# Kernel tuning notes

Hardware: AMD Instinct MI355X
Metric: run time of the kernel (lower is better)

The kernel has to match this reference:

```python
import jax, jax.numpy as jnp
import numpy as np

N_NODES = 100_000
N_EDGES = 1_000_000
IN_CH = 32
EDGE_CH = 16
OUT_CH = 32
D_CAT = 2 * IN_CH + EDGE_CH  # 80
D_MID = 56                   # linspace(80, 32, 3)[1]


def setup_inputs() -> dict:
    key = jax.random.key(0)
    ks = jax.random.split(key, 8)
    x = jax.random.normal(ks[0], (N_NODES, IN_CH), dtype=jnp.float32)
    edge_index = jax.random.randint(ks[1], (2, N_EDGES), 0, N_NODES, dtype=jnp.int64)
    edge_attr = jax.random.normal(ks[2], (N_EDGES, EDGE_CH), dtype=jnp.float32)
    # MLP params: Linear(80->56), Linear(56->32), bias=True (homogeneous_flag=False)
    W1 = jax.random.normal(ks[3], (D_CAT, D_MID), dtype=jnp.float32) / np.sqrt(D_CAT).astype(np.float32)
    b1 = jnp.zeros((D_MID,), dtype=jnp.float32)
    W2 = jax.random.normal(ks[4], (D_MID, OUT_CH), dtype=jnp.float32) / np.sqrt(D_MID).astype(np.float32)
    b2 = jnp.zeros((OUT_CH,), dtype=jnp.float32)
    return {"x": x, "edge_index": edge_index, "edge_attr": edge_attr,
            "W1": W1, "b1": b1, "W2": W2, "b2": b2}


def reference(x, edge_index, edge_attr, W1, b1, W2, b2):
    num_nodes = x.shape[0]
    rol, col = edge_index[0], edge_index[1]
    # gather node pairs + concat edge features: [E, 2*in + edge]
    e = jnp.concatenate([x[rol], x[col], edge_attr], axis=-1)
    # edge MLP (LeakyReLU after every layer, as in IterGNN's MLP)
    h = jax.nn.leaky_relu(e @ W1 + b1)
    v = jax.nn.leaky_relu(h @ W2 + b2)  # [E, out]
    # Max aggregation by destination node (scatter-max); empty segments -> 0
    agg = jax.ops.segment_max(v, col, num_segments=num_nodes)
    agg = jnp.where(jnp.isneginf(agg), jnp.zeros((), dtype=agg.dtype), agg)
    # elementwise max with trailing slice of input features
    out = jnp.maximum(agg, x[:, -v.shape[-1]:])
    return out
```

## Files before the change

### kernel.cpp

```cpp
#include <hip/hip_runtime.h>

#define N_NODES 100000
#define IN_CH 32
#define EDGE_CH 16
#define OUT_CH 32
#define D_CAT 80
#define D_MID 56

#define BKT_SHIFT 6
#define BKT_NODES 64
#define NB 1563
#define NB_ALL 1568
#define CAP 1024

#define NSUP 196
#define CAP_SUP 5632
#define K1_EDGES 2048
#define K1_EPT 4
#define K2_SPLIT 4
#define K2_SLICE 1408
#define K2_SITERS 3

#define EPB 256
#define NT_E 16

#define W1F_SH 4096
#define W2F_SH 2048
#define W1D_SH 2048
#define WIMG_SH (W1F_SH + W2F_SH + W1D_SH)
#define FEATF_SH (NT_E * 2 * 64 * 8)

#define HSTRIDE 68
#define AGG_LD 33
#define ENC_NEGINF 0x007FFFFFu

typedef short short8 __attribute__((ext_vector_type(8)));
typedef float f32x4 __attribute__((ext_vector_type(4)));
typedef int i32x2 __attribute__((ext_vector_type(2)));

#define WS_IMG    0
#define WS_B1     16384
#define WS_B2     16640
#define WS_SUPCNT 16768
#define WS_GCNT   17664
#define WS_Z0     16768
#define WS_ZSZ    (17664 + 6272 - 16768)
#define WS_SUPREC 24576
#define WS_REC    8855552
#define WS_XB_A   21700608
#define XB_BYTES  6400000
#define WS_NEED_A ((size_t)WS_XB_A)
#define WS_NEED_AX ((size_t)WS_XB_A + XB_BYTES)
#define WS_XB_B   12869632
#define WS_NEED_B ((size_t)WS_XB_B)
#define WS_NEED_BX ((size_t)WS_XB_B + XB_BYTES)

__device__ __forceinline__ unsigned fenc(float f) {
    unsigned u = __float_as_uint(f);
    return (u & 0x80000000u) ? ~u : (u | 0x80000000u);
}
__device__ __forceinline__ float fdec(unsigned u) {
    u = (u & 0x80000000u) ? (u ^ 0x80000000u) : ~u;
    return __uint_as_float(u);
}
__device__ __forceinline__ float bfr(float f) {
    unsigned u = __float_as_uint(f);
    u = (u + 0x7FFFu + ((u >> 16) & 1u)) & 0xFFFF0000u;
    return __uint_as_float(u);
}
__device__ __forceinline__ unsigned short bf16b(float f) {
    unsigned u = __float_as_uint(f);
    return (unsigned short)((u + 0x7FFFu + ((u >> 16) & 1u)) >> 16);
}
__device__ __forceinline__ short8 cvt8(float4 a, float4 b) {
    return short8{ (short)bf16b(a.x), (short)bf16b(a.y), (short)bf16b(a.z), (short)bf16b(a.w),
                   (short)bf16b(b.x), (short)bf16b(b.y), (short)bf16b(b.z), (short)bf16b(b.w) };
}

__device__ __forceinline__ void convert_x_bf16(const float* __restrict__ x,
                                               unsigned short* __restrict__ xb,
                                               int gtid, int gstride) {
    const int tot = N_NODES * IN_CH / 8;
    for (int i = gtid; i < tot; i += gstride) {
        float4 a = ((const float4*)x)[2 * i];
        float4 b = ((const float4*)x)[2 * i + 1];
        *(short8*)&xb[i * 8] = cvt8(a, b);
    }
}

__device__ void build_weight_image(const float* __restrict__ W1, const float* __restrict__ b1,
                                   const float* __restrict__ W2, const float* __restrict__ b2,
                                   unsigned short* __restrict__ wsImg,
                                   float* __restrict__ wsb1, float* __restrict__ wsb2,
                                   int t, int nthr) {
    for (int s = t; s < W1F_SH; s += nthr) {
        int j = s & 7, l = (s >> 3) & 63, fi = s >> 9;
        int nt = fi & 3, ks = fi >> 2;
        int n = nt * 16 + (l & 15), kl = ks * 32 + (l >> 4) * 8 + j;
        unsigned short v = 0;
        if (n < D_MID) {
            if (kl < 32) v = bf16b(W1[kl * D_MID + n]);
            else if (kl < 48) v = bf16b(W1[(64 + kl - 32) * D_MID + n]);
        }
        wsImg[s] = v;
    }
    for (int s = t; s < W2F_SH; s += nthr) {
        int j = s & 7, l = (s >> 3) & 63, fi = s >> 9;
        int nt = fi & 1, ks = fi >> 1;
        int n = nt * 16 + (l & 15), kl = ks * 32 + (l >> 4) * 8 + j;
        wsImg[W1F_SH + s] = (kl < D_MID) ? bf16b(W2[kl * OUT_CH + n]) : (unsigned short)0;
    }
    for (int s = t; s < W1D_SH; s += nthr) {
        int j = s & 7, l = (s >> 3) & 63, fi = s >> 9;
        int nt = fi & 3;
        int n = nt * 16 + (l & 15), kl = (l >> 4) * 8 + j;
        wsImg[W1F_SH + W2F_SH + s] = (n < D_MID) ? bf16b(W1[(32 + kl) * D_MID + n]) : (unsigned short)0;
    }
    if (t < 64) wsb1[t] = (t < D_MID) ? bfr(b1[t]) : 0.f;
    else if (t < 96) wsb2[t - 64] = bfr(b2[t - 64]);
}

__global__ __launch_bounds__(512) void coarse_bin(
    const int* __restrict__ ei, int nE, int* __restrict__ gSupCnt, int2* __restrict__ supRec,
    const float* __restrict__ W1, const float* __restrict__ b1,
    const float* __restrict__ W2, const float* __restrict__ b2,
    unsigned short* __restrict__ wsImg, float* __restrict__ wsb1, float* __restrict__ wsb2)
{
    __shared__ int cnt[256], wb[256], cur[256];
    const int t = threadIdx.x;
    if (blockIdx.x == 0) build_weight_image(W1, b1, W2, b2, wsImg, wsb1, wsb2, t, 512);
    if (t < 256) cnt[t] = 0;
    __syncthreads();

    const int lo = blockIdx.x * K1_EDGES;
    int rdst[K1_EPT], rsrc[K1_EPT];
#pragma unroll
    for (int k = 0; k < K1_EPT; ++k) {
        int e = lo + k * 512 + t;
        bool v = e < nE;
        rdst[k] = v ? __builtin_nontemporal_load(ei + nE + e) : -1;
        rsrc[k] = v ? __builtin_nontemporal_load(ei + e) : 0;
        if ((unsigned)rdst[k] >= N_NODES) rdst[k] = -1;
        if ((unsigned)rsrc[k] >= N_NODES) rsrc[k] = 0;
        if (rdst[k] >= 0) atomicAdd(&cnt[rdst[k] >> 9], 1);
    }
    __syncthreads();
    if (t < 256) {
        int c = cnt[t];
        wb[t] = c ? atomicAdd(&gSupCnt[t], c) : 0;
        cur[t] = 0;
    }
    __syncthreads();
#pragma unroll
    for (int k = 0; k < K1_EPT; ++k) {
        if (rdst[k] >= 0) {
            int s = rdst[k] >> 9;
            int pos = wb[s] + atomicAdd(&cur[s], 1);
            if (pos < CAP_SUP) {
                int e = lo + k * 512 + t;
                supRec[(size_t)s * CAP_SUP + pos] =
                    make_int2(rsrc[k], ((rdst[k] & 511) << 20) | e);
            }
        }
    }
}

__global__ __launch_bounds__(512) void fine_bin(
    const int* __restrict__ gSupCnt, const int2* __restrict__ supRec,
    int* __restrict__ gCnt, int2* __restrict__ rec,
    const float* __restrict__ x, unsigned short* __restrict__ xb)
{
    const int blk = blockIdx.x;
    const int s = blk >> 2, sl = blk & (K2_SPLIT - 1);
    const int t = threadIdx.x, lane = t & 63;

    if (xb) convert_x_bf16(x, xb, blk * 512 + t, NSUP * K2_SPLIT * 512);

    const int cntS = min(gSupCnt[s], CAP_SUP);
    const int lo = sl * K2_SLICE;
    const int hi = min(cntS, lo + K2_SLICE);

    int2 r[K2_SITERS];
#pragma unroll
    for (int k = 0; k < K2_SITERS; ++k) {
        int i = lo + k * 512 + t;
        r[k] = (i < hi) ? supRec[(size_t)s * CAP_SUP + i] : make_int2(0, 0);
    }
#pragma unroll
    for (int k = 0; k < K2_SITERS; ++k) {
        int i = lo + k * 512 + t;
        bool v = i < hi;
        int f = v ? ((r[k].y >> 26) & 7) : -1;
        int rank = 0, wbase = 0;
#pragma unroll
        for (int vv = 0; vv < 8; ++vv) {
            unsigned long long m = __ballot(f == vv);
            if (lane == vv) wbase = m ? atomicAdd(&gCnt[s * 8 + vv], (int)__popcll(m)) : 0;
            if (f == vv) rank = (int)__popcll(m & ((1ull << lane) - 1ull));
        }
        int base = __shfl(wbase, f & 7);
        if (v) {
            int pos = base + rank;
            if (pos < CAP)
                rec[(size_t)(s * 8 + f) * CAP + pos] =
                    make_int2(r[k].x, (((r[k].y >> 20) & 63) << 20) | (r[k].y & 0xFFFFF));
        }
    }
}

__global__ __launch_bounds__(512) void scatter_append(
    const int* __restrict__ ei, int* __restrict__ gCnt, int2* __restrict__ rec, int nE,
    const float* __restrict__ W1, const float* __restrict__ b1,
    const float* __restrict__ W2, const float* __restrict__ b2,
    unsigned short* __restrict__ wsImg, float* __restrict__ wsb1, float* __restrict__ wsb2,
    const float* __restrict__ x, unsigned short* __restrict__ xb)
{
    __shared__ int lh[NB];
    __shared__ int lbase[NB];
    if (blockIdx.x == 0) build_weight_image(W1, b1, W2, b2, wsImg, wsb1, wsb2, threadIdx.x, 512);
    if (xb) convert_x_bf16(x, xb, blockIdx.x * 512 + threadIdx.x, gridDim.x * 512);
    for (int i = threadIdx.x; i < NB; i += 512) lh[i] = 0;
    __syncthreads();
    int per = (nE + gridDim.x - 1) / gridDim.x;
    int lo = blockIdx.x * per;
    int hi = min(lo + per, nE);
    for (int e = lo + threadIdx.x; e < hi; e += 512) {
        int dst = __builtin_nontemporal_load(ei + nE + e);
        if ((unsigned)dst < N_NODES) atomicAdd(&lh[dst >> BKT_SHIFT], 1);
    }
    __syncthreads();
    for (int i = threadIdx.x; i < NB; i += 512) {
        int c = lh[i];
        lbase[i] = c ? atomicAdd(&gCnt[i], c) : 0;
        lh[i] = 0;
    }
    __syncthreads();
    for (int e = lo + threadIdx.x; e < hi; e += 512) {
        int dst = __builtin_nontemporal_load(ei + nE + e);
        if ((unsigned)dst >= N_NODES) continue;
        int b = dst >> BKT_SHIFT;
        int p = lbase[b] + atomicAdd(&lh[b], 1);
        if (p >= CAP) continue;
        int src = __builtin_nontemporal_load(ei + e);
        if ((unsigned)src >= N_NODES) src = 0;
        rec[(size_t)b * CAP + p] = make_int2(src, ((dst & (BKT_NODES - 1)) << 20) | e);
    }
}

template<int XB>
__global__ __launch_bounds__(512, 4) void bucket_mlp(
    const float* __restrict__ x, const unsigned short* __restrict__ xb,
    const float* __restrict__ ea,
    const int2* __restrict__ rec, const int* __restrict__ gCnt,
    const unsigned short* __restrict__ wsImg,
    const float* __restrict__ wsb1, const float* __restrict__ wsb2,
    float* __restrict__ out)
{
    __shared__ unsigned short sFeatF[FEATF_SH];
    __shared__ unsigned short sWgt[WIMG_SH];
    __shared__ float sHdst[BKT_NODES * HSTRIDE];
    __shared__ unsigned aggL[BKT_NODES * AGG_LD];
    __shared__ float sb1f[64];
    __shared__ float sb2f[32];
    __shared__ int sdl[EPB];

    unsigned short* const sW1F = sWgt;
    unsigned short* const sW2F = sWgt + W1F_SH;
    unsigned short* const sW1D = sWgt + W1F_SH + W2F_SH;
    unsigned short* const sHF  = sFeatF;

    const int t = threadIdx.x;
    const int nodeBase = blockIdx.x << BKT_SHIFT;
    const int base = blockIdx.x * CAP;
    const int cnt  = min(gCnt[blockIdx.x], CAP);

    for (int i = t; i < WIMG_SH / 8; i += 512)
        *(short8*)&sWgt[i * 8] = *(const short8*)(wsImg + i * 8);
    for (int i = t; i < BKT_NODES * AGG_LD; i += 512) aggL[i] = ENC_NEGINF;
    if (t < 64) sb1f[t] = wsb1[t];
    else if (t < 96) sb2f[t - 64] = wsb2[t - 64];

    const int wave = t >> 6;
    const int l15  = t & 15;
    const int quad = (t & 63) >> 4;
    const int lane = t & 63;
    const int slot = t >> 1, q = t & 1;
    const int sl15 = slot & 15, set = slot >> 4;

    short8 rv16[4];
    int rdl;

    auto loadRec = [&](int idx) -> i32x2 {
        return (idx < cnt) ? *(const i32x2*)(rec + base + idx) : (i32x2){0, 0};
    };
    auto gather = [&](i32x2 r2, bool ok) {
        rdl = ok ? ((r2.y >> 20) & 63) : -1;
        short8 z = {0, 0, 0, 0, 0, 0, 0, 0};
        if (q == 0) {
            if constexpr (XB) {
                const short8* xs8 = (const short8*)(xb + (size_t)r2.x * IN_CH);
#pragma unroll
                for (int k = 0; k < 4; ++k) rv16[k] = ok ? xs8[k] : z;
            } else {
                const float* xs = x + (size_t)r2.x * IN_CH;
#pragma unroll
                for (int k = 0; k < 4; ++k)
                    rv16[k] = ok ? cvt8(((const float4*)xs)[2 * k], ((const float4*)xs)[2 * k + 1]) : z;
            }
        } else {
            const float* ep = ea + (size_t)(r2.y & 0xFFFFF) * EDGE_CH;
#pragma unroll
            for (int k = 0; k < 2; ++k)
                rv16[k] = ok ? cvt8(((const float4*)ep)[2 * k], ((const float4*)ep)[2 * k + 1]) : z;
            rv16[2] = z; rv16[3] = z;
        }
    };
    auto storeChunk = [&]() {
        if (q == 0) sdl[slot] = rdl;
#pragma unroll
        for (int k = 0; k < 4; ++k) {
            int cj = q * 4 + k;
            int a16 = (set * 2 + (cj >> 2)) * 64 + (cj & 3) * 16 + sl15;
            *(short8*)&sFeatF[a16 * 8] = rv16[k];
        }
    };

    i32x2 recC = loadRec(slot);
    i32x2 recN = loadRec(EPB + slot);
    gather(recC, slot < cnt);

    __syncthreads();

    {
        const int ntile = wave & 3, mh = wave >> 2;
        int node = nodeBase + ntile * 16 + l15;
        short8 bfr8 = {0, 0, 0, 0, 0, 0, 0, 0};
        if (node < N_NODES) {
            if constexpr (XB) {
                bfr8 = *(const short8*)(xb + (size_t)node * IN_CH + quad * 8);
            } else {
                const float* xp = x + (size_t)node * IN_CH + quad * 8;
                bfr8 = cvt8(((const float4*)xp)[0], ((const float4*)xp)[1]);
            }
        }
        f32x4 accd[2] = {(f32x4){0.f, 0.f, 0.f, 0.f}, (f32x4){0.f, 0.f, 0.f, 0.f}};
#pragma unroll
        for (int i = 0; i < 2; ++i) {
            int nt = mh * 2 + i;
            short8 af = *(const short8*)&sW1D[(nt * 64 + lane) * 8];
            accd[i] = __builtin_amdgcn_mfma_f32_16x16x32_bf16(af, bfr8, accd[i], 0, 0, 0);
        }
#pragma unroll
        for (int i = 0; i < 2; ++i) {
            int nt = mh * 2 + i, c0 = nt * 16 + quad * 4;
            float4 vv;
#pragma unroll
            for (int j = 0; j < 4; ++j) {
                int c = c0 + j;
                ((float*)&vv)[j] = (c < D_MID) ? accd[i][j] + sb1f[c] : 0.f;
            }
            *(float4*)&sHdst[(ntile * 16 + l15) * HSTRIDE + c0] = vv;
        }
    }

    for (int c0e = 0; c0e < cnt; c0e += EPB) {
        storeChunk();
        __syncthreads();
        gather(recN, (c0e + EPB + slot) < cnt);
        recN = loadRec(c0e + 2 * EPB + slot);

        f32x4 acc[2][4];
#pragma unroll
        for (int ei = 0; ei < 2; ++ei)
#pragma unroll
            for (int nt = 0; nt < 4; ++nt) acc[ei][nt] = (f32x4){0.f, 0.f, 0.f, 0.f};
#pragma unroll
        for (int ks = 0; ks < 2; ++ks) {
            short8 bf0 = *(const short8*)&sFeatF[((wave * 2 + ks) * 64 + lane) * 8];
            short8 bf1 = *(const short8*)&sFeatF[(((wave + 8) * 2 + ks) * 64 + lane) * 8];
#pragma unroll
            for (int nt = 0; nt < 4; ++nt) {
                short8 af = *(const short8*)&sW1F[((ks * 4 + nt) * 64 + lane) * 8];
                acc[0][nt] = __builtin_amdgcn_mfma_f32_16x16x32_bf16(af, bf0, acc[0][nt], 0, 0, 0);
                acc[1][nt] = __builtin_amdgcn_mfma_f32_16x16x32_bf16(af, bf1, acc[1][nt], 0, 0, 0);
            }
        }
        __syncthreads();

#pragma unroll
        for (int ei = 0; ei < 2; ++ei) {
            int et = wave + ei * 8;
            int dl = sdl[et * 16 + l15];
            const float* hrow = &sHdst[((dl >= 0) ? dl : 0) * HSTRIDE];
#pragma unroll
            for (int nt = 0; nt < 4; ++nt) {
                int c0 = nt * 16 + quad * 4;
                float4 hd = *(const float4*)&hrow[c0];
                int ks2 = nt >> 1;
                int quad2 = (nt * 2 + (quad >> 1)) & 3;
                int off = (quad & 1) * 4;
                ushort4 p;
#pragma unroll
                for (int j = 0; j < 4; ++j) {
                    float v = acc[ei][nt][j] + ((const float*)&hd)[j];
                    v = (v > 0.f) ? v : 0.01f * v;
                    ((unsigned short*)&p)[j] = (c0 + j < D_MID) ? bf16b(v) : (unsigned short)0;
                }
                *(ushort4*)&sHF[((et * 2 + ks2) * 64 + quad2 * 16 + l15) * 8 + off] = p;
            }
        }
        __syncthreads();

        f32x4 acc2[2][2];
#pragma unroll
        for (int ei = 0; ei < 2; ++ei)
#pragma unroll
            for (int nt = 0; nt < 2; ++nt) acc2[ei][nt] = (f32x4){0.f, 0.f, 0.f, 0.f};
#pragma unroll
        for (int ks = 0; ks < 2; ++ks) {
            short8 bf0 = *(const short8*)&sHF[((wave * 2 + ks) * 64 + lane) * 8];
            short8 bf1 = *(const short8*)&sHF[(((wave + 8) * 2 + ks) * 64 + lane) * 8];
#pragma unroll
            for (int nt = 0; nt < 2; ++nt) {
                short8 af = *(const short8*)&sW2F[((ks * 2 + nt) * 64 + lane) * 8];
                acc2[0][nt] = __builtin_amdgcn_mfma_f32_16x16x32_bf16(af, bf0, acc2[0][nt], 0, 0, 0);
                acc2[1][nt] = __builtin_amdgcn_mfma_f32_16x16x32_bf16(af, bf1, acc2[1][nt], 0, 0, 0);
            }
        }

#pragma unroll
        for (int ei = 0; ei < 2; ++ei) {
            int et = wave + ei * 8;
            int dl = sdl[et * 16 + l15];
            if (dl >= 0) {
                unsigned* arow = &aggL[dl * AGG_LD];
#pragma unroll
                for (int nt = 0; nt < 2; ++nt) {
                    int c0 = nt * 16 + quad * 4;
#pragma unroll
                    for (int j = 0; j < 4; ++j) {
                        float v = acc2[ei][nt][j] + sb2f[c0 + j];
                        v = (v > 0.f) ? v : 0.01f * v;
                        atomicMax(arow + c0 + j, fenc(bfr(v)));
                    }
                }
            }
        }
        __syncthreads();
    }
    __syncthreads();

    {
        int nl = t >> 3, g4 = t & 7;
        int node = nodeBase + nl;
        if (node < N_NODES) {
            const unsigned* ar = &aggL[nl * AGG_LD + g4 * 4];
            float4 o;
            if constexpr (XB) {
                ushort4 xw = ((const ushort4*)(xb + (size_t)node * IN_CH))[g4];
                o.x = fmaxf((ar[0] == ENC_NEGINF) ? 0.f : fdec(ar[0]), __uint_as_float((unsigned)xw.x << 16));
                o.y = fmaxf((ar[1] == ENC_NEGINF) ? 0.f : fdec(ar[1]), __uint_as_float((unsigned)xw.y << 16));
                o.z = fmaxf((ar[2] == ENC_NEGINF) ? 0.f : fdec(ar[2]), __uint_as_float((unsigned)xw.z << 16));
                o.w = fmaxf((ar[3] == ENC_NEGINF) ? 0.f : fdec(ar[3]), __uint_as_float((unsigned)xw.w << 16));
            } else {
                float4 xv = ((const float4*)(x + (size_t)node * IN_CH))[g4];
                o.x = fmaxf((ar[0] == ENC_NEGINF) ? 0.f : fdec(ar[0]), bfr(xv.x));
                o.y = fmaxf((ar[1] == ENC_NEGINF) ? 0.f : fdec(ar[1]), bfr(xv.y));
                o.z = fmaxf((ar[2] == ENC_NEGINF) ? 0.f : fdec(ar[2]), bfr(xv.z));
                o.w = fmaxf((ar[3] == ENC_NEGINF) ? 0.f : fdec(ar[3]), bfr(xv.w));
            }
            ((float4*)(out + (size_t)node * OUT_CH))[g4] = o;
        }
    }
}

extern "C" void kernel_launch(void* const* d_in, const int* in_sizes, int n_in,
                              void* d_out, int out_size, void* d_ws, size_t ws_size,
                              hipStream_t stream) {
    const float* x  = (const float*)d_in[0];
    const int*   ei = (const int*)d_in[1];
    const float* ea = (const float*)d_in[2];
    const float* W1 = (const float*)d_in[3];
    const float* b1 = (const float*)d_in[4];
    const float* W2 = (const float*)d_in[5];
    const float* b2 = (const float*)d_in[6];

    char* ws = (char*)d_ws;
    unsigned short* wsImg = (unsigned short*)(ws + WS_IMG);
    float* wsb1 = (float*)(ws + WS_B1);
    float* wsb2 = (float*)(ws + WS_B2);
    int* gSupCnt = (int*)(ws + WS_SUPCNT);
    int* gCnt = (int*)(ws + WS_GCNT);

    const int nE = in_sizes[1] / 2;
    float* out = (float*)d_out;

    if (ws_size >= WS_NEED_A) {
        int2* supRec = (int2*)(ws + WS_SUPREC);
        int2* rec    = (int2*)(ws + WS_REC);
        bool xbOn = ws_size >= WS_NEED_AX;
        unsigned short* xb = xbOn ? (unsigned short*)(ws + WS_XB_A) : nullptr;
        hipMemsetAsync(ws + WS_Z0, 0, WS_ZSZ, stream);
        coarse_bin<<<(nE + K1_EDGES - 1) / K1_EDGES, 512, 0, stream>>>(
            ei, nE, gSupCnt, supRec, W1, b1, W2, b2, wsImg, wsb1, wsb2);
        fine_bin<<<NSUP * K2_SPLIT, 512, 0, stream>>>(gSupCnt, supRec, gCnt, rec, x, xb);
        if (xbOn)
            bucket_mlp<1><<<NB, 512, 0, stream>>>(x, xb, ea, rec, gCnt, wsImg, wsb1, wsb2, out);
        else
            bucket_mlp<0><<<NB, 512, 0, stream>>>(x, nullptr, ea, rec, gCnt, wsImg, wsb1, wsb2, out);
    } else {
        int2* rec = (int2*)(ws + 24576);
        bool xbOn = ws_size >= WS_NEED_BX;
        unsigned short* xb = xbOn ? (unsigned short*)(ws + WS_XB_B) : nullptr;
        hipMemsetAsync(gCnt, 0, NB_ALL * sizeof(int), stream);
        scatter_append<<<128, 512, 0, stream>>>(ei, gCnt, rec, nE, W1, b1, W2, b2,
                                                wsImg, wsb1, wsb2, x, xb);
        if (xbOn)
            bucket_mlp<1><<<NB, 512, 0, stream>>>(x, xb, ea, rec, gCnt, wsImg, wsb1, wsb2, out);
        else
            bucket_mlp<0><<<NB, 512, 0, stream>>>(x, nullptr, ea, rec, gCnt, wsImg, wsb1, wsb2, out);
    }
}
```

Before: 225.2 us.

## Fuse edge binning and bucket MLP into one cooperative kernel with grid sync

Adds a cooperative kernel that first bins edges into destination buckets with block-local histograms and global atomics. After a grid-wide sync, the same persistent blocks loop over the buckets and run the bf16 MFMA edge MLP with scatter-max aggregation. The launcher tries this path first and falls back to the old multi-kernel pipelines if the cooperative launch fails. This removes the separate coarse and fine binning passes and the inter-kernel launch gaps. In exchange it relies on a fixed grid of 512 persistent blocks, adds grid-sync cost, and gives up the two-level binning's write locality.

```diff
diff --git a/kernel.cpp b/kernel.cpp
--- a/kernel.cpp
+++ b/kernel.cpp
@@ -1,4 +1,7 @@
 #include <hip/hip_runtime.h>
+#include <hip/hip_cooperative_groups.h>
+
+namespace cg = cooperative_groups;
 
 #define N_NODES 100000
 #define IN_CH 32
@@ -20,6 +23,8 @@
 #define K2_SPLIT 4
 #define K2_SLICE 1408
 #define K2_SITERS 3
+
+#define COOP_GRID 512
 
 #define EPB 256
 #define NT_E 16
@@ -120,6 +125,281 @@
     else if (t < 96) wsb2[t - 64] = bfr(b2[t - 64]);
 }
 
+template<int XB>
+__global__ __launch_bounds__(512, 4) void fused_all(
+    const float* __restrict__ x, unsigned short* __restrict__ xb,
+    const float* __restrict__ ea, const int* __restrict__ ei, int nE,
+    int* __restrict__ gCnt, int2* __restrict__ rec,
+    const float* __restrict__ W1, const float* __restrict__ b1,
+    const float* __restrict__ W2, const float* __restrict__ b2,
+    unsigned short* __restrict__ wsImg, float* __restrict__ wsb1, float* __restrict__ wsb2,
+    float* __restrict__ out)
+{
+    __shared__ unsigned short sFeatF[FEATF_SH];
+    __shared__ unsigned short sWgt[WIMG_SH];
+    __shared__ float sHdst[BKT_NODES * HSTRIDE];
+    __shared__ unsigned aggL[BKT_NODES * AGG_LD];
+    __shared__ float sb1f[64];
+    __shared__ float sb2f[32];
+    __shared__ int sdl[EPB];
+
+    const int t = threadIdx.x;
+    const int blk = blockIdx.x, nblk = gridDim.x;
+
+    {
+        int* const lh = (int*)sFeatF;
+        int* const lbase = ((int*)sFeatF) + NB;
+        if (blk == 0) build_weight_image(W1, b1, W2, b2, wsImg, wsb1, wsb2, t, 512);
+        if constexpr (XB) convert_x_bf16(x, xb, blk * 512 + t, nblk * 512);
+        for (int i = t; i < NB; i += 512) lh[i] = 0;
+        __syncthreads();
+
+        const int per = (nE + nblk - 1) / nblk;
+        const int lo = blk * per, hi = min(lo + per, nE);
+        int rdst[4], rsrc[4];
+#pragma unroll
+        for (int k = 0; k < 4; ++k) {
+            int e = lo + k * 512 + t;
+            bool v = e < hi;
+            rdst[k] = v ? __builtin_nontemporal_load(ei + nE + e) : -1;
+            rsrc[k] = v ? __builtin_nontemporal_load(ei + e) : 0;
+            if ((unsigned)rdst[k] >= N_NODES) rdst[k] = -1;
+            if ((unsigned)rsrc[k] >= N_NODES) rsrc[k] = 0;
+            if (rdst[k] >= 0) atomicAdd(&lh[rdst[k] >> BKT_SHIFT], 1);
+        }
+        __syncthreads();
+        for (int i = t; i < NB; i += 512) {
+            int c = lh[i];
+            lbase[i] = c ? atomicAdd(&gCnt[i], c) : 0;
+            lh[i] = 0;
+        }
+        __syncthreads();
+#pragma unroll
+        for (int k = 0; k < 4; ++k) {
+            if (rdst[k] >= 0) {
+                int b = rdst[k] >> BKT_SHIFT;
+                int p = lbase[b] + atomicAdd(&lh[b], 1);
+                if (p < CAP) {
+                    int e = lo + k * 512 + t;
+                    rec[(size_t)b * CAP + p] = make_int2(rsrc[k], ((rdst[k] & 63) << 20) | e);
+                }
+            }
+        }
+    }
+
+    cg::this_grid().sync();
+
+    unsigned short* const sW1F = sWgt;
+    unsigned short* const sW2F = sWgt + W1F_SH;
+    unsigned short* const sW1D = sWgt + W1F_SH + W2F_SH;
+    unsigned short* const sHF  = sFeatF;
+
+    for (int i = t; i < WIMG_SH / 8; i += 512)
+        *(short8*)&sWgt[i * 8] = *(const short8*)(wsImg + i * 8);
+    if (t < 64) sb1f[t] = wsb1[t];
+    else if (t < 96) sb2f[t - 64] = wsb2[t - 64];
+
+    const int wave = t >> 6;
+    const int l15  = t & 15;
+    const int quad = (t & 63) >> 4;
+    const int lane = t & 63;
+    const int slot = t >> 1, q = t & 1;
+    const int sl15 = slot & 15, set = slot >> 4;
+
+    for (int b = blk; b < NB; b += nblk) {
+        const int nodeBase = b << BKT_SHIFT;
+        const int base = b * CAP;
+        const int cnt  = min(gCnt[b], CAP);
+
+        __syncthreads();
+        for (int i = t; i < BKT_NODES * AGG_LD; i += 512) aggL[i] = ENC_NEGINF;
+
+        short8 rv16[4];
+        int rdl;
+        auto loadRec = [&](int idx) -> i32x2 {
+            return (idx < cnt) ? *(const i32x2*)(rec + base + idx) : (i32x2){0, 0};
+        };
+        auto gather = [&](i32x2 r2, bool ok) {
+            rdl = ok ? ((r2.y >> 20) & 63) : -1;
+            short8 z = {0, 0, 0, 0, 0, 0, 0, 0};
+            if (q == 0) {
+                if constexpr (XB) {
+                    const short8* xs8 = (const short8*)(xb + (size_t)r2.x * IN_CH);
+#pragma unroll
+                    for (int k = 0; k < 4; ++k) rv16[k] = ok ? xs8[k] : z;
+                } else {
+                    const float* xs = x + (size_t)r2.x * IN_CH;
+#pragma unroll
+                    for (int k = 0; k < 4; ++k)
+                        rv16[k] = ok ? cvt8(((const float4*)xs)[2 * k], ((const float4*)xs)[2 * k + 1]) : z;
+                }
+            } else {
+                const float* ep = ea + (size_t)(r2.y & 0xFFFFF) * EDGE_CH;
+#pragma unroll
+                for (int k = 0; k < 2; ++k)
+                    rv16[k] = ok ? cvt8(((const float4*)ep)[2 * k], ((const float4*)ep)[2 * k + 1]) : z;
+                rv16[2] = z; rv16[3] = z;
+            }
+        };
+        auto storeChunk = [&]() {
+            if (q == 0) sdl[slot] = rdl;
+#pragma unroll
+            for (int k = 0; k < 4; ++k) {
+                int cj = q * 4 + k;
+                int a16 = (set * 2 + (cj >> 2)) * 64 + (cj & 3) * 16 + sl15;
+                *(short8*)&sFeatF[a16 * 8] = rv16[k];
+            }
+        };
+
+        i32x2 recC = loadRec(slot);
+        i32x2 recN = loadRec(EPB + slot);
+        gather(recC, slot < cnt);
+
+        {
+            const int ntile = wave & 3, mh = wave >> 2;
+            int node = nodeBase + ntile * 16 + l15;
+            short8 bfr8 = {0, 0, 0, 0, 0, 0, 0, 0};
+            if (node < N_NODES) {
+                if constexpr (XB) {
+                    bfr8 = *(const short8*)(xb + (size_t)node * IN_CH + quad * 8);
+                } else {
+                    const float* xp = x + (size_t)node * IN_CH + quad * 8;
+                    bfr8 = cvt8(((const float4*)xp)[0], ((const float4*)xp)[1]);
+                }
+            }
+            f32x4 accd[2] = {(f32x4){0.f, 0.f, 0.f, 0.f}, (f32x4){0.f, 0.f, 0.f, 0.f}};
+#pragma unroll
+            for (int i = 0; i < 2; ++i) {
+                int nt = mh * 2 + i;
+                short8 af = *(const short8*)&sW1D[(nt * 64 + lane) * 8];
+                accd[i] = __builtin_amdgcn_mfma_f32_16x16x32_bf16(af, bfr8, accd[i], 0, 0, 0);
+            }
+#pragma unroll
+            for (int i = 0; i < 2; ++i) {
+                int nt = mh * 2 + i, c0 = nt * 16 + quad * 4;
+                float4 vv;
+#pragma unroll
+                for (int j = 0; j < 4; ++j) {
+                    int c = c0 + j;
+                    ((float*)&vv)[j] = (c < D_MID) ? accd[i][j] + sb1f[c] : 0.f;
+                }
+                *(float4*)&sHdst[(ntile * 16 + l15) * HSTRIDE + c0] = vv;
+            }
+        }
+
+        for (int c0e = 0; c0e < cnt; c0e += EPB) {
+            storeChunk();
+            __syncthreads();
+            gather(recN, (c0e + EPB + slot) < cnt);
+            recN = loadRec(c0e + 2 * EPB + slot);
+
+            f32x4 acc[2][4];
+#pragma unroll
+            for (int ei2 = 0; ei2 < 2; ++ei2)
+#pragma unroll
+                for (int nt = 0; nt < 4; ++nt) acc[ei2][nt] = (f32x4){0.f, 0.f, 0.f, 0.f};
+#pragma unroll
+            for (int ks = 0; ks < 2; ++ks) {
+                short8 bf0 = *(const short8*)&sFeatF[((wave * 2 + ks) * 64 + lane) * 8];
+                short8 bf1 = *(const short8*)&sFeatF[(((wave + 8) * 2 + ks) * 64 + lane) * 8];
+#pragma unroll
+                for (int nt = 0; nt < 4; ++nt) {
+                    short8 af = *(const short8*)&sW1F[((ks * 4 + nt) * 64 + lane) * 8];
+                    acc[0][nt] = __builtin_amdgcn_mfma_f32_16x16x32_bf16(af, bf0, acc[0][nt], 0, 0, 0);
+                    acc[1][nt] = __builtin_amdgcn_mfma_f32_16x16x32_bf16(af, bf1, acc[1][nt], 0, 0, 0);
+                }
+            }
+            __syncthreads();
+
+#pragma unroll
+            for (int ei2 = 0; ei2 < 2; ++ei2) {
+                int et = wave + ei2 * 8;
+                int dl = sdl[et * 16 + l15];
+                const float* hrow = &sHdst[((dl >= 0) ? dl : 0) * HSTRIDE];
+#pragma unroll
+                for (int nt = 0; nt < 4; ++nt) {
+                    int c0 = nt * 16 + quad * 4;
+                    float4 hd = *(const float4*)&hrow[c0];
+                    int ks2 = nt >> 1;
+                    int quad2 = (nt * 2 + (quad >> 1)) & 3;
+                    int off = (quad & 1) * 4;
+                    ushort4 p;
+#pragma unroll
+                    for (int j = 0; j < 4; ++j) {
+                        float v = acc[ei2][nt][j] + ((const float*)&hd)[j];
+                        v = (v > 0.f) ? v : 0.01f * v;
+                        ((unsigned short*)&p)[j] = (c0 + j < D_MID) ? bf16b(v) : (unsigned short)0;
+                    }
+                    *(ushort4*)&sHF[((et * 2 + ks2) * 64 + quad2 * 16 + l15) * 8 + off] = p;
+                }
+            }
+            __syncthreads();
+
+            f32x4 acc2[2][2];
+#pragma unroll
+            for (int ei2 = 0; ei2 < 2; ++ei2)
+#pragma unroll
+                for (int nt = 0; nt < 2; ++nt) acc2[ei2][nt] = (f32x4){0.f, 0.f, 0.f, 0.f};
+#pragma unroll
+            for (int ks = 0; ks < 2; ++ks) {
+                short8 bf0 = *(const short8*)&sHF[((wave * 2 + ks) * 64 + lane) * 8];
+                short8 bf1 = *(const short8*)&sHF[(((wave + 8) * 2 + ks) * 64 + lane) * 8];
+#pragma unroll
+                for (int nt = 0; nt < 2; ++nt) {
+                    short8 af = *(const short8*)&sW2F[((ks * 2 + nt) * 64 + lane) * 8];
+                    acc2[0][nt] = __builtin_amdgcn_mfma_f32_16x16x32_bf16(af, bf0, acc2[0][nt], 0, 0, 0);
+                    acc2[1][nt] = __builtin_amdgcn_mfma_f32_16x16x32_bf16(af, bf1, acc2[1][nt], 0, 0, 0);
+                }
+            }
+
+#pragma unroll
+            for (int ei2 = 0; ei2 < 2; ++ei2) {
+                int et = wave + ei2 * 8;
+                int dl = sdl[et * 16 + l15];
+                if (dl >= 0) {
+                    unsigned* arow = &aggL[dl * AGG_LD];
+#pragma unroll
+                    for (int nt = 0; nt < 2; ++nt) {
+                        int c0 = nt * 16 + quad * 4;
+#pragma unroll
+                        for (int j = 0; j < 4; ++j) {
+                            float v = acc2[ei2][nt][j] + sb2f[c0 + j];
+                            v = (v > 0.f) ? v : 0.01f * v;
+                            atomicMax(arow + c0 + j, fenc(bfr(v)));
+                        }
+                    }
+                }
+            }
+            __syncthreads();
+        }
+        __syncthreads();
+
+        {
+            int nl = t >> 3, g4 = t & 7;
+            int node = nodeBase + nl;
+            if (node < N_NODES) {
+                const unsigned* ar = &aggL[nl * AGG_LD + g4 * 4];
+                float4 o;
+                if constexpr (XB) {
+                    ushort4 xw = ((const ushort4*)(xb + (size_t)node * IN_CH))[g4];
+                    o.x = fmaxf((ar[0] == ENC_NEGINF) ? 0.f : fdec(ar[0]), __uint_as_float((unsigned)xw.x << 16));
+                    o.y = fmaxf((ar[1] == ENC_NEGINF) ? 0.f : fdec(ar[1]), __uint_as_float((unsigned)xw.y << 16));
+                    o.z = fmaxf((ar[2] == ENC_NEGINF) ? 0.f : fdec(ar[2]), __uint_as_float((unsigned)xw.z << 16));
+                    o.w = fmaxf((ar[3] == ENC_NEGINF) ? 0.f : fdec(ar[3]), __uint_as_float((unsigned)xw.w << 16));
+                } else {
+                    float4 xv = ((const float4*)(x + (size_t)node * IN_CH))[g4];
+                    o.x = fmaxf((ar[0] == ENC_NEGINF) ? 0.f : fdec(ar[0]), bfr(xv.x));
+                    o.y = fmaxf((ar[1] == ENC_NEGINF) ? 0.f : fdec(ar[1]), bfr(xv.y));
+                    o.z = fmaxf((ar[2] == ENC_NEGINF) ? 0.f : fdec(ar[2]), bfr(xv.z));
+                    o.w = fmaxf((ar[3] == ENC_NEGINF) ? 0.f : fdec(ar[3]), bfr(xv.w));
+                }
+                ((float4*)(out + (size_t)node * OUT_CH))[g4] = o;
+            }
+        }
+    }
+}
+
+
 __global__ __launch_bounds__(512) void coarse_bin(
     const int* __restrict__ ei, int nE, int* __restrict__ gSupCnt, int2* __restrict__ supRec,
     const float* __restrict__ W1, const float* __restrict__ b1,
@@ -204,6 +484,233 @@
             if (pos < CAP)
                 rec[(size_t)(s * 8 + f) * CAP + pos] =
                     make_int2(r[k].x, (((r[k].y >> 20) & 63) << 20) | (r[k].y & 0xFFFFF));
+        }
+    }
+}
+
+template<int XB>
+__global__ __launch_bounds__(512, 4) void bucket_mlp(
+    const float* __restrict__ x, const unsigned short* __restrict__ xb,
+    const float* __restrict__ ea,
+    const int2* __restrict__ rec, const int* __restrict__ gCnt,
+    const unsigned short* __restrict__ wsImg,
+    const float* __restrict__ wsb1, const float* __restrict__ wsb2,
+    float* __restrict__ out)
+{
+    __shared__ unsigned short sFeatF[FEATF_SH];
+    __shared__ unsigned short sWgt[WIMG_SH];
+    __shared__ float sHdst[BKT_NODES * HSTRIDE];
+    __shared__ unsigned aggL[BKT_NODES * AGG_LD];
+    __shared__ float sb1f[64];
+    __shared__ float sb2f[32];
+    __shared__ int sdl[EPB];
+
+    unsigned short* const sW1F = sWgt;
+    unsigned short* const sW2F = sWgt + W1F_SH;
+    unsigned short* const sW1D = sWgt + W1F_SH + W2F_SH;
+    unsigned short* const sHF  = sFeatF;
+
+    const int t = threadIdx.x;
+    const int nodeBase = blockIdx.x << BKT_SHIFT;
+    const int base = blockIdx.x * CAP;
+    const int cnt  = min(gCnt[blockIdx.x], CAP);
+
+    for (int i = t; i < WIMG_SH / 8; i += 512)
+        *(short8*)&sWgt[i * 8] = *(const short8*)(wsImg + i * 8);
+    for (int i = t; i < BKT_NODES * AGG_LD; i += 512) aggL[i] = ENC_NEGINF;
+    if (t < 64) sb1f[t] = wsb1[t];
+    else if (t < 96) sb2f[t - 64] = wsb2[t - 64];
+
+    const int wave = t >> 6;
+    const int l15  = t & 15;
+    const int quad = (t & 63) >> 4;
+    const int lane = t & 63;
+    const int slot = t >> 1, q = t & 1;
+    const int sl15 = slot & 15, set = slot >> 4;
+
+    short8 rv16[4];
+    int rdl;
+
+    auto loadRec = [&](int idx) -> i32x2 {
+        return (idx < cnt) ? *(const i32x2*)(rec + base + idx) : (i32x2){0, 0};
+    };
+    auto gather = [&](i32x2 r2, bool ok) {
+        rdl = ok ? ((r2.y >> 20) & 63) : -1;
+        short8 z = {0, 0, 0, 0, 0, 0, 0, 0};
+        if (q == 0) {
+            if constexpr (XB) {
+                const short8* xs8 = (const short8*)(xb + (size_t)r2.x * IN_CH);
+#pragma unroll
+                for (int k = 0; k < 4; ++k) rv16[k] = ok ? xs8[k] : z;
+            } else {
+                const float* xs = x + (size_t)r2.x * IN_CH;
+#pragma unroll
+                for (int k = 0; k < 4; ++k)
+                    rv16[k] = ok ? cvt8(((const float4*)xs)[2 * k], ((const float4*)xs)[2 * k + 1]) : z;
+            }
+        } else {
+            const float* ep = ea + (size_t)(r2.y & 0xFFFFF) * EDGE_CH;
+#pragma unroll
+            for (int k = 0; k < 2; ++k)
+                rv16[k] = ok ? cvt8(((const float4*)ep)[2 * k], ((const float4*)ep)[2 * k + 1]) : z;
+            rv16[2] = z; rv16[3] = z;
+        }
+    };
+    auto storeChunk = [&]() {
+        if (q == 0) sdl[slot] = rdl;
+#pragma unroll
+        for (int k = 0; k < 4; ++k) {
+            int cj = q * 4 + k;
+            int a16 = (set * 2 + (cj >> 2)) * 64 + (cj & 3) * 16 + sl15;
+            *(short8*)&sFeatF[a16 * 8] = rv16[k];
+        }
+    };
+
+    i32x2 recC = loadRec(slot);
+    i32x2 recN = loadRec(EPB + slot);
+    gather(recC, slot < cnt);
+
+    __syncthreads();
+
+    {
+        const int ntile = wave & 3, mh = wave >> 2;
+        int node = nodeBase + ntile * 16 + l15;
+        short8 bfr8 = {0, 0, 0, 0, 0, 0, 0, 0};
+        if (node < N_NODES) {
+            if constexpr (XB) {
+                bfr8 = *(const short8*)(xb + (size_t)node * IN_CH + quad * 8);
+            } else {
+                const float* xp = x + (size_t)node * IN_CH + quad * 8;
+                bfr8 = cvt8(((const float4*)xp)[0], ((const float4*)xp)[1]);
+            }
+        }
+        f32x4 accd[2] = {(f32x4){0.f, 0.f, 0.f, 0.f}, (f32x4){0.f, 0.f, 0.f, 0.f}};
+#pragma unroll
+        for (int i = 0; i < 2; ++i) {
+            int nt = mh * 2 + i;
+            short8 af = *(const short8*)&sW1D[(nt * 64 + lane) * 8];
+            accd[i] = __builtin_amdgcn_mfma_f32_16x16x32_bf16(af, bfr8, accd[i], 0, 0, 0);
+        }
+#pragma unroll
+        for (int i = 0; i < 2; ++i) {
+            int nt = mh * 2 + i, c0 = nt * 16 + quad * 4;
+            float4 vv;
+#pragma unroll
+            for (int j = 0; j < 4; ++j) {
+                int c = c0 + j;
+                ((float*)&vv)[j] = (c < D_MID) ? accd[i][j] + sb1f[c] : 0.f;
+            }
+            *(float4*)&sHdst[(ntile * 16 + l15) * HSTRIDE + c0] = vv;
+        }
+    }
+
+    for (int c0e = 0; c0e < cnt; c0e += EPB) {
+        storeChunk();
+        __syncthreads();
+        gather(recN, (c0e + EPB + slot) < cnt);
+        recN = loadRec(c0e + 2 * EPB + slot);
+
+        f32x4 acc[2][4];
+#pragma unroll
+        for (int ei2 = 0; ei2 < 2; ++ei2)
+#pragma unroll
+            for (int nt = 0; nt < 4; ++nt) acc[ei2][nt] = (f32x4){0.f, 0.f, 0.f, 0.f};
+#pragma unroll
+        for (int ks = 0; ks < 2; ++ks) {
+            short8 bf0 = *(const short8*)&sFeatF[((wave * 2 + ks) * 64 + lane) * 8];
+            short8 bf1 = *(const short8*)&sFeatF[(((wave + 8) * 2 + ks) * 64 + lane) * 8];
+#pragma unroll
+            for (int nt = 0; nt < 4; ++nt) {
+                short8 af = *(const short8*)&sW1F[((ks * 4 + nt) * 64 + lane) * 8];
+                acc[0][nt] = __builtin_amdgcn_mfma_f32_16x16x32_bf16(af, bf0, acc[0][nt], 0, 0, 0);
+                acc[1][nt] = __builtin_amdgcn_mfma_f32_16x16x32_bf16(af, bf1, acc[1][nt], 0, 0, 0);
+            }
+        }
+        __syncthreads();
+
+#pragma unroll
+        for (int ei2 = 0; ei2 < 2; ++ei2) {
+            int et = wave + ei2 * 8;
+            int dl = sdl[et * 16 + l15];
+            const float* hrow = &sHdst[((dl >= 0) ? dl : 0) * HSTRIDE];
+#pragma unroll
+            for (int nt = 0; nt < 4; ++nt) {
+                int c0 = nt * 16 + quad * 4;
+                float4 hd = *(const float4*)&hrow[c0];
+                int ks2 = nt >> 1;
+                int quad2 = (nt * 2 + (quad >> 1)) & 3;
+                int off = (quad & 1) * 4;
+                ushort4 p;
+#pragma unroll
+                for (int j = 0; j < 4; ++j) {
+                    float v = acc[ei2][nt][j] + ((const float*)&hd)[j];
+                    v = (v > 0.f) ? v : 0.01f * v;
+                    ((unsigned short*)&p)[j] = (c0 + j < D_MID) ? bf16b(v) : (unsigned short)0;
+                }
+                *(ushort4*)&sHF[((et * 2 + ks2) * 64 + quad2 * 16 + l15) * 8 + off] = p;
+            }
+        }
+        __syncthreads();
+
+        f32x4 acc2[2][2];
+#pragma unroll
+        for (int ei2 = 0; ei2 < 2; ++ei2)
+#pragma unroll
+            for (int nt = 0; nt < 2; ++nt) acc2[ei2][nt] = (f32x4){0.f, 0.f, 0.f, 0.f};
+#pragma unroll
+        for (int ks = 0; ks < 2; ++ks) {
+            short8 bf0 = *(const short8*)&sHF[((wave * 2 + ks) * 64 + lane) * 8];
+            short8 bf1 = *(const short8*)&sHF[(((wave + 8) * 2 + ks) * 64 + lane) * 8];
+#pragma unroll
+            for (int nt = 0; nt < 2; ++nt) {
+                short8 af = *(const short8*)&sW2F[((ks * 2 + nt) * 64 + lane) * 8];
+                acc2[0][nt] = __builtin_amdgcn_mfma_f32_16x16x32_bf16(af, bf0, acc2[0][nt], 0, 0, 0);
+                acc2[1][nt] = __builtin_amdgcn_mfma_f32_16x16x32_bf16(af, bf1, acc2[1][nt], 0, 0, 0);
+            }
+        }
+
+#pragma unroll
+        for (int ei2 = 0; ei2 < 2; ++ei2) {
+            int et = wave + ei2 * 8;
+            int dl = sdl[et * 16 + l15];
+            if (dl >= 0) {
+                unsigned* arow = &aggL[dl * AGG_LD];
+#pragma unroll
+                for (int nt = 0; nt < 2; ++nt) {
+                    int c0 = nt * 16 + quad * 4;
+#pragma unroll
+                    for (int j = 0; j < 4; ++j) {
+                        float v = acc2[ei2][nt][j] + sb2f[c0 + j];
+                        v = (v > 0.f) ? v : 0.01f * v;
+                        atomicMax(arow + c0 + j, fenc(bfr(v)));
+                    }
+                }
+            }
+        }
+        __syncthreads();
+    }
+    __syncthreads();
+
+    {
+        int nl = t >> 3, g4 = t & 7;
+        int node = nodeBase + nl;
+        if (node < N_NODES) {
+            const unsigned* ar = &aggL[nl * AGG_LD + g4 * 4];
+            float4 o;
+            if constexpr (XB) {
+                ushort4 xw = ((const ushort4*)(xb + (size_t)node * IN_CH))[g4];
+                o.x = fmaxf((ar[0] == ENC_NEGINF) ? 0.f : fdec(ar[0]), __uint_as_float((unsigned)xw.x << 16));
+                o.y = fmaxf((ar[1] == ENC_NEGINF) ? 0.f : fdec(ar[1]), __uint_as_float((unsigned)xw.y << 16));
+                o.z = fmaxf((ar[2] == ENC_NEGINF) ? 0.f : fdec(ar[2]), __uint_as_float((unsigned)xw.z << 16));
+                o.w = fmaxf((ar[3] == ENC_NEGINF) ? 0.f : fdec(ar[3]), __uint_as_float((unsigned)xw.w << 16));
+            } else {
+                float4 xv = ((const float4*)(x + (size_t)node * IN_CH))[g4];
+                o.x = fmaxf((ar[0] == ENC_NEGINF) ? 0.f : fdec(ar[0]), bfr(xv.x));
+                o.y = fmaxf((ar[1] == ENC_NEGINF) ? 0.f : fdec(ar[1]), bfr(xv.y));
+                o.z = fmaxf((ar[2] == ENC_NEGINF) ? 0.f : fdec(ar[2]), bfr(xv.z));
+                o.w = fmaxf((ar[3] == ENC_NEGINF) ? 0.f : fdec(ar[3]), bfr(xv.w));
+            }
+            ((float4*)(out + (size_t)node * OUT_CH))[g4] = o;
         }
     }
 }
@@ -247,233 +754,6 @@
     }
 }
 
-template<int XB>
-__global__ __launch_bounds__(512, 4) void bucket_mlp(
-    const float* __restrict__ x, const unsigned short* __restrict__ xb,
-    const float* __restrict__ ea,
-    const int2* __restrict__ rec, const int* __restrict__ gCnt,
-    const unsigned short* __restrict__ wsImg,
-    const float* __restrict__ wsb1, const float* __restrict__ wsb2,
-    float* __restrict__ out)
-{
-    __shared__ unsigned short sFeatF[FEATF_SH];
-    __shared__ unsigned short sWgt[WIMG_SH];
-    __shared__ float sHdst[BKT_NODES * HSTRIDE];
-    __shared__ unsigned aggL[BKT_NODES * AGG_LD];
-    __shared__ float sb1f[64];
-    __shared__ float sb2f[32];
-    __shared__ int sdl[EPB];
-
-    unsigned short* const sW1F = sWgt;
-    unsigned short* const sW2F = sWgt + W1F_SH;
-    unsigned short* const sW1D = sWgt + W1F_SH + W2F_SH;
-    unsigned short* const sHF  = sFeatF;
-
-    const int t = threadIdx.x;
-    const int nodeBase = blockIdx.x << BKT_SHIFT;
-    const int base = blockIdx.x * CAP;
-    const int cnt  = min(gCnt[blockIdx.x], CAP);
-
-    for (int i = t; i < WIMG_SH / 8; i += 512)
-        *(short8*)&sWgt[i * 8] = *(const short8*)(wsImg + i * 8);
-    for (int i = t; i < BKT_NODES * AGG_LD; i += 512) aggL[i] = ENC_NEGINF;
-    if (t < 64) sb1f[t] = wsb1[t];
-    else if (t < 96) sb2f[t - 64] = wsb2[t - 64];
-
-    const int wave = t >> 6;
-    const int l15  = t & 15;
-    const int quad = (t & 63) >> 4;
-    const int lane = t & 63;
-    const int slot = t >> 1, q = t & 1;
-    const int sl15 = slot & 15, set = slot >> 4;
-
-    short8 rv16[4];
-    int rdl;
-
-    auto loadRec = [&](int idx) -> i32x2 {
-        return (idx < cnt) ? *(const i32x2*)(rec + base + idx) : (i32x2){0, 0};
-    };
-    auto gather = [&](i32x2 r2, bool ok) {
-        rdl = ok ? ((r2.y >> 20) & 63) : -1;
-        short8 z = {0, 0, 0, 0, 0, 0, 0, 0};
-        if (q == 0) {
-            if constexpr (XB) {
-                const short8* xs8 = (const short8*)(xb + (size_t)r2.x * IN_CH);
-#pragma unroll
-                for (int k = 0; k < 4; ++k) rv16[k] = ok ? xs8[k] : z;
-            } else {
-                const float* xs = x + (size_t)r2.x * IN_CH;
-#pragma unroll
-                for (int k = 0; k < 4; ++k)
-                    rv16[k] = ok ? cvt8(((const float4*)xs)[2 * k], ((const float4*)xs)[2 * k + 1]) : z;
-            }
-        } else {
-            const float* ep = ea + (size_t)(r2.y & 0xFFFFF) * EDGE_CH;
-#pragma unroll
-            for (int k = 0; k < 2; ++k)
-                rv16[k] = ok ? cvt8(((const float4*)ep)[2 * k], ((const float4*)ep)[2 * k + 1]) : z;
-            rv16[2] = z; rv16[3] = z;
-        }
-    };
-    auto storeChunk = [&]() {
-        if (q == 0) sdl[slot] = rdl;
-#pragma unroll
-        for (int k = 0; k < 4; ++k) {
-            int cj = q * 4 + k;
-            int a16 = (set * 2 + (cj >> 2)) * 64 + (cj & 3) * 16 + sl15;
-            *(short8*)&sFeatF[a16 * 8] = rv16[k];
-        }
-    };
-
-    i32x2 recC = loadRec(slot);
-    i32x2 recN = loadRec(EPB + slot);
-    gather(recC, slot < cnt);
-
-    __syncthreads();
-
-    {
-        const int ntile = wave & 3, mh = wave >> 2;
-        int node = nodeBase + ntile * 16 + l15;
-        short8 bfr8 = {0, 0, 0, 0, 0, 0, 0, 0};
-        if (node < N_NODES) {
-            if constexpr (XB) {
-                bfr8 = *(const short8*)(xb + (size_t)node * IN_CH + quad * 8);
-            } else {
-                const float* xp = x + (size_t)node * IN_CH + quad * 8;
-                bfr8 = cvt8(((const float4*)xp)[0], ((const float4*)xp)[1]);
-            }
-        }
-        f32x4 accd[2] = {(f32x4){0.f, 0.f, 0.f, 0.f}, (f32x4){0.f, 0.f, 0.f, 0.f}};
-#pragma unroll
-        for (int i = 0; i < 2; ++i) {
-            int nt = mh * 2 + i;
-            short8 af = *(const short8*)&sW1D[(nt * 64 + lane) * 8];
-            accd[i] = __builtin_amdgcn_mfma_f32_16x16x32_bf16(af, bfr8, accd[i], 0, 0, 0);
-        }
-#pragma unroll
-        for (int i = 0; i < 2; ++i) {
-            int nt = mh * 2 + i, c0 = nt * 16 + quad * 4;
-            float4 vv;
-#pragma unroll
-            for (int j = 0; j < 4; ++j) {
-                int c = c0 + j;
-                ((float*)&vv)[j] = (c < D_MID) ? accd[i][j] + sb1f[c] : 0.f;
-            }
-            *(float4*)&sHdst[(ntile * 16 + l15) * HSTRIDE + c0] = vv;
-        }
-    }
-
-    for (int c0e = 0; c0e < cnt; c0e += EPB) {
-        storeChunk();
-        __syncthreads();
-        gather(recN, (c0e + EPB + slot) < cnt);
-        recN = loadRec(c0e + 2 * EPB + slot);
-
-        f32x4 acc[2][4];
-#pragma unroll
-        for (int ei = 0; ei < 2; ++ei)
-#pragma unroll
-            for (int nt = 0; nt < 4; ++nt) acc[ei][nt] = (f32x4){0.f, 0.f, 0.f, 0.f};
-#pragma unroll
-        for (int ks = 0; ks < 2; ++ks) {
-            short8 bf0 = *(const short8*)&sFeatF[((wave * 2 + ks) * 64 + lane) * 8];
-            short8 bf1 = *(const short8*)&sFeatF[(((wave + 8) * 2 + ks) * 64 + lane) * 8];
-#pragma unroll
-            for (int nt = 0; nt < 4; ++nt) {
-                short8 af = *(const short8*)&sW1F[((ks * 4 + nt) * 64 + lane) * 8];
-                acc[0][nt] = __builtin_amdgcn_mfma_f32_16x16x32_bf16(af, bf0, acc[0][nt], 0, 0, 0);
-                acc[1][nt] = __builtin_amdgcn_mfma_f32_16x16x32_bf16(af, bf1, acc[1][nt], 0, 0, 0);
-            }
-        }
-        __syncthreads();
-
-#pragma unroll
-        for (int ei = 0; ei < 2; ++ei) {
-            int et = wave + ei * 8;
-            int dl = sdl[et * 16 + l15];
-            const float* hrow = &sHdst[((dl >= 0) ? dl : 0) * HSTRIDE];
-#pragma unroll
-            for (int nt = 0; nt < 4; ++nt) {
-                int c0 = nt * 16 + quad * 4;
-                float4 hd = *(const float4*)&hrow[c0];
-                int ks2 = nt >> 1;
-                int quad2 = (nt * 2 + (quad >> 1)) & 3;
-                int off = (quad & 1) * 4;
-                ushort4 p;
-#pragma unroll
-                for (int j = 0; j < 4; ++j) {
-                    float v = acc[ei][nt][j] + ((const float*)&hd)[j];
-                    v = (v > 0.f) ? v : 0.01f * v;
-                    ((unsigned short*)&p)[j] = (c0 + j < D_MID) ? bf16b(v) : (unsigned short)0;
-                }
-                *(ushort4*)&sHF[((et * 2 + ks2) * 64 + quad2 * 16 + l15) * 8 + off] = p;
-            }
-        }
-        __syncthreads();
-
-        f32x4 acc2[2][2];
-#pragma unroll
-        for (int ei = 0; ei < 2; ++ei)
-#pragma unroll
-            for (int nt = 0; nt < 2; ++nt) acc2[ei][nt] = (f32x4){0.f, 0.f, 0.f, 0.f};
-#pragma unroll
-        for (int ks = 0; ks < 2; ++ks) {
-            short8 bf0 = *(const short8*)&sHF[((wave * 2 + ks) * 64 + lane) * 8];
-            short8 bf1 = *(const short8*)&sHF[(((wave + 8) * 2 + ks) * 64 + lane) * 8];
-#pragma unroll
-            for (int nt = 0; nt < 2; ++nt) {
-                short8 af = *(const short8*)&sW2F[((ks * 2 + nt) * 64 + lane) * 8];
-                acc2[0][nt] = __builtin_amdgcn_mfma_f32_16x16x32_bf16(af, bf0, acc2[0][nt], 0, 0, 0);
-                acc2[1][nt] = __builtin_amdgcn_mfma_f32_16x16x32_bf16(af, bf1, acc2[1][nt], 0, 0, 0);
-            }
-        }
-
-#pragma unroll
-        for (int ei = 0; ei < 2; ++ei) {
-            int et = wave + ei * 8;
-            int dl = sdl[et * 16 + l15];
-            if (dl >= 0) {
-                unsigned* arow = &aggL[dl * AGG_LD];
-#pragma unroll
-                for (int nt = 0; nt < 2; ++nt) {
-                    int c0 = nt * 16 + quad * 4;
-#pragma unroll
-                    for (int j = 0; j < 4; ++j) {
-                        float v = acc2[ei][nt][j] + sb2f[c0 + j];
-                        v = (v > 0.f) ? v : 0.01f * v;
-                        atomicMax(arow + c0 + j, fenc(bfr(v)));
-                    }
-                }
-            }
-        }
-        __syncthreads();
-    }
-    __syncthreads();
-
-    {
-        int nl = t >> 3, g4 = t & 7;
-        int node = nodeBase + nl;
-        if (node < N_NODES) {
-            const unsigned* ar = &aggL[nl * AGG_LD + g4 * 4];
-            float4 o;
-            if constexpr (XB) {
-                ushort4 xw = ((const ushort4*)(xb + (size_t)node * IN_CH))[g4];
-                o.x = fmaxf((ar[0] == ENC_NEGINF) ? 0.f : fdec(ar[0]), __uint_as_float((unsigned)xw.x << 16));
-                o.y = fmaxf((ar[1] == ENC_NEGINF) ? 0.f : fdec(ar[1]), __uint_as_float((unsigned)xw.y << 16));
-                o.z = fmaxf((ar[2] == ENC_NEGINF) ? 0.f : fdec(ar[2]), __uint_as_float((unsigned)xw.z << 16));
-                o.w = fmaxf((ar[3] == ENC_NEGINF) ? 0.f : fdec(ar[3]), __uint_as_float((unsigned)xw.w << 16));
-            } else {
-                float4 xv = ((const float4*)(x + (size_t)node * IN_CH))[g4];
-                o.x = fmaxf((ar[0] == ENC_NEGINF) ? 0.f : fdec(ar[0]), bfr(xv.x));
-                o.y = fmaxf((ar[1] == ENC_NEGINF) ? 0.f : fdec(ar[1]), bfr(xv.y));
-                o.z = fmaxf((ar[2] == ENC_NEGINF) ? 0.f : fdec(ar[2]), bfr(xv.z));
-                o.w = fmaxf((ar[3] == ENC_NEGINF) ? 0.f : fdec(ar[3]), bfr(xv.w));
-            }
-            ((float4*)(out + (size_t)node * OUT_CH))[g4] = o;
-        }
-    }
-}
-
 extern "C" void kernel_launch(void* const* d_in, const int* in_sizes, int n_in,
                               void* d_out, int out_size, void* d_ws, size_t ws_size,
                               hipStream_t stream) {
@@ -494,6 +774,22 @@
 
     const int nE = in_sizes[1] / 2;
     float* out = (float*)d_out;
+
+    if (ws_size >= WS_NEED_B) {
+        int2* rec = (int2*)(ws + 24576);
+        bool xbOn = ws_size >= WS_NEED_BX;
+        unsigned short* xb = xbOn ? (unsigned short*)(ws + WS_XB_B) : nullptr;
+        hipMemsetAsync(gCnt, 0, NB_ALL * sizeof(int), stream);
+        void* args[] = {(void*)&x, (void*)&xb, (void*)&ea, (void*)&ei, (void*)&nE,
+                        (void*)&gCnt, (void*)&rec, (void*)&W1, (void*)&b1, (void*)&W2,
+                        (void*)&b2, (void*)&wsImg, (void*)&wsb1, (void*)&wsb2, (void*)&out};
+        const void* kfn = xbOn ? reinterpret_cast<const void*>(fused_all<1>)
+                               : reinterpret_cast<const void*>(fused_all<0>);
+        hipError_t err = hipLaunchCooperativeKernel(kfn, dim3(COOP_GRID), dim3(512),
+                                                    args, 0, stream);
+        if (err == hipSuccess) return;
+        (void)hipGetLastError();
+    }
 
     if (ws_size >= WS_NEED_A) {
         int2* supRec = (int2*)(ws + WS_SUPREC);
```

New measurement: 276.3 us. +22.7%, slower.
